# Optimization experiments

Measured on AMD Instinct MI355X. Metric: run time of the kernel, lower is better.

The kernel has to match this reference:

```python
import jax, jax.numpy as jnp
import numpy as np

STATE = 256
HYPER = 256
QHID = 64
NAGENTS = 8


def _lin_init(key, fan_in, fan_out):
    # torch nn.Linear default init: U(-1/sqrt(fan_in), 1/sqrt(fan_in))
    kw, kb = jax.random.split(key)
    bound = 1.0 / np.sqrt(fan_in)
    W = jax.random.uniform(kw, (fan_in, fan_out), jnp.float32, -bound, bound)
    b = jax.random.uniform(kb, (fan_out,), jnp.float32, -bound, bound)
    return W, b


def setup_inputs() -> dict:
    key = jax.random.key(0)
    ks = jax.random.split(key, 8)
    q_value_batch = jax.random.normal(ks[0], (128, 512, NAGENTS, 1), jnp.float32)
    state_batch = jax.random.normal(ks[1], (128, 512, 1, STATE), jnp.float32)
    W1a, b1a = _lin_init(ks[2], STATE, HYPER)
    W1b, b1b = _lin_init(ks[3], HYPER, NAGENTS * QHID)
    W2a, b2a = _lin_init(ks[4], STATE, HYPER)
    W2b, b2b = _lin_init(ks[5], HYPER, QHID)
    Wb1, bb1 = _lin_init(ks[6], STATE, QHID)
    kb2a, kb2b = jax.random.split(ks[7])
    Wb2a, bb2a = _lin_init(kb2a, STATE, QHID)
    Wb2b, bb2b = _lin_init(kb2b, QHID, 1)
    return {
        "q_value_batch": q_value_batch, "state_batch": state_batch,
        "W1a": W1a, "b1a": b1a, "W1b": W1b, "b1b": b1b,
        "W2a": W2a, "b2a": b2a, "W2b": W2b, "b2b": b2b,
        "Wb1": Wb1, "bb1": bb1,
        "Wb2a": Wb2a, "bb2a": bb2a, "Wb2b": Wb2b, "bb2b": bb2b,
    }


def reference(q_value_batch, state_batch,
              W1a, b1a, W1b, b1b,
              W2a, b2a, W2b, b2b,
              Wb1, bb1, Wb2a, bb2a, Wb2b, bb2b):
    B = q_value_batch.shape[0]
    # flatten (num_episode, episode_limit) -> N
    q = q_value_batch.reshape(-1, 1, NAGENTS)          # [N, 1, A]
    s = state_batch.reshape(-1, STATE)                 # [N, S]
    # hypernet w1: S -> H -> A*Q, abs
    w1 = jnp.abs(jax.nn.relu(s @ W1a + b1a) @ W1b + b1b)
    w1 = w1.reshape(-1, NAGENTS, QHID)                 # [N, A, Q]
    b1 = (s @ Wb1 + bb1)[:, None, :]                   # [N, 1, Q]
    hidden = jax.nn.elu(jnp.einsum('nxa,naq->nxq', q, w1) + b1)  # [N, 1, Q]
    # hypernet w2: S -> H -> Q, abs
    w2 = jnp.abs(jax.nn.relu(s @ W2a + b2a) @ W2b + b2b)[:, :, None]  # [N, Q, 1]
    b2 = (jax.nn.relu(s @ Wb2a + bb2a) @ Wb2b + bb2b)[:, :, None]     # [N, 1, 1]
    q_total = jnp.einsum('nxq,nqo->nxo', hidden, w2) + b2             # [N, 1, 1]
    return q_total.reshape(B, -1, 1)
```

## Files before the change

### kernel.cpp

```cpp
#include <hip/hip_runtime.h>

typedef __bf16 bf16_t;
typedef bf16_t bf16x8 __attribute__((ext_vector_type(8)));
typedef bf16_t bf16x4 __attribute__((ext_vector_type(4)));
typedef bf16_t bf16x2 __attribute__((ext_vector_type(2)));
typedef float f32x4 __attribute__((ext_vector_type(4)));

#define MFMA __builtin_amdgcn_mfma_f32_16x16x32_bf16
#define SWZ(row, off) ((off) ^ (((row) & 7) << 4))

#define OFF_W1AT   0
#define OFF_W2AT   65536
#define OFF_W1BT   131072
#define OFF_SMALLT 262144
#define OFF_W2BT   294912
#define OFF_W2OUT  622592ul
#define OFF_B1ROW  9011200ul
#define OFF_B2OUT  17399808ul

__device__ __forceinline__ bf16x8 cvt8(float4 a, float4 b) {
  bf16x8 v;
  v[0]=(bf16_t)a.x; v[1]=(bf16_t)a.y; v[2]=(bf16_t)a.z; v[3]=(bf16_t)a.w;
  v[4]=(bf16_t)b.x; v[5]=(bf16_t)b.y; v[6]=(bf16_t)b.z; v[7]=(bf16_t)b.w;
  return v;
}

__global__ __launch_bounds__(256) void cvt_wT(
    const float* __restrict__ W1a, const float* __restrict__ W2a,
    const float* __restrict__ W1b, const float* __restrict__ Wb1,
    const float* __restrict__ Wb2a, const float* __restrict__ W2b,
    bf16_t* __restrict__ ws)
{
  int gid = blockIdx.x * 256 + threadIdx.x;
  const float* src; int base, nout;
  if (gid < 65536)       { src = W1a;  base = 0;      nout = 256; }
  else if (gid < 131072) { src = W2a;  base = 65536;  nout = 256; }
  else if (gid < 262144) { src = W1b;  base = 131072; nout = 512; }
  else if (gid < 278528) { src = Wb1;  base = 262144; nout = 64;  }
  else if (gid < 294912) { src = Wb2a; base = 278528; nout = 64;  }
  else                   { src = W2b;  base = 294912; nout = 64;  }
  int local = gid - base, col = local >> 8, k = local & 255;
  ws[gid] = (bf16_t)src[k * nout + col];
}

__global__ __launch_bounds__(512) void qmix_k1(
    const float* __restrict__ s, const bf16_t* __restrict__ ws,
    const float* __restrict__ b2a, const float* __restrict__ b2b,
    const float* __restrict__ bb1, const float* __restrict__ bb2a,
    const float* __restrict__ Wb2b, const float* __restrict__ bb2b,
    bf16_t* __restrict__ w2out, bf16_t* __restrict__ b1row,
    float* __restrict__ b2out)
{
  __shared__ __align__(16) char ldsV[64 * 512];
  __shared__ __align__(16) char sT[2][16 * 512];
  __shared__ __align__(16) char h2T[16 * 512];
  __shared__ float b2part[4][16];

  const int tid = threadIdx.x, wave = tid >> 6, lane = tid & 63;
  const int r16 = lane & 15, g = lane >> 4;
  const int row0 = blockIdx.x * 128;
  const int srow = tid >> 5, sc = tid & 31;

  bf16x8 aW[2][8], aSm[8];
  {
    const bf16_t* w2aT = ws + OFF_W2AT;
    const bf16_t* smT  = ws + OFF_SMALLT;
    #pragma unroll
    for (int t = 0; t < 2; ++t) {
      int col = (wave + t * 8) * 16 + r16;
      #pragma unroll
      for (int kk = 0; kk < 8; ++kk)
        aW[t][kk] = *(const bf16x8*)(w2aT + col * 256 + kk * 32 + g * 8);
    }
    int scol = wave * 16 + r16;
    #pragma unroll
    for (int kk = 0; kk < 8; ++kk)
      aSm[kk] = *(const bf16x8*)(smT + scol * 256 + kk * 32 + g * 8);
  }
  {
    const char* src = (const char*)(ws + OFF_W2BT);
    for (int c = tid; c < 2048; c += 512) {
      int col = c >> 5, o = (c & 31) * 16;
      *(float4*)(&ldsV[col * 512 + SWZ(col, o)]) = *(const float4*)(src + c * 16);
    }
  }
  {
    const float* p = s + (size_t)(row0 + srow) * 256 + sc * 8;
    float4 f0 = *(const float4*)p, f1 = *(const float4*)(p + 4);
    *(bf16x8*)(&sT[0][srow * 512 + SWZ(srow, sc * 16)]) = cvt8(f0, f1);
  }
  __syncthreads();

  for (int rt = 0; rt < 8; ++rt) {
    const int cur = rt & 1;
    const int rowt = row0 + rt * 16;
    float4 pf0, pf1;
    if (rt < 7) {
      const float* p = s + (size_t)(rowt + 16 + srow) * 256 + sc * 8;
      pf0 = *(const float4*)p; pf1 = *(const float4*)(p + 4);
    }
    f32x4 acc0 = (f32x4)0.f, acc1 = (f32x4)0.f, accS = (f32x4)0.f;
    #pragma unroll
    for (int kk = 0; kk < 8; ++kk) {
      bf16x8 sB = *(const bf16x8*)(&sT[cur][r16 * 512 + SWZ(r16, kk * 64 + g * 16)]);
      acc0 = MFMA(aW[0][kk], sB, acc0, 0, 0, 0);
      acc1 = MFMA(aW[1][kk], sB, acc1, 0, 0, 0);
      accS = MFMA(aSm[kk], sB, accS, 0, 0, 0);
    }
    if (wave < 4) {
      float4 bb = *(const float4*)(bb1 + wave * 16 + 4 * g);
      bf16x4 o;
      o[0]=(bf16_t)(accS[0]+bb.x); o[1]=(bf16_t)(accS[1]+bb.y);
      o[2]=(bf16_t)(accS[2]+bb.z); o[3]=(bf16_t)(accS[3]+bb.w);
      *(bf16x4*)(b1row + (size_t)(rowt + r16) * 64 + wave * 16 + 4 * g) = o;
    } else {
      float4 ba = *(const float4*)(bb2a + (wave - 4) * 16 + 4 * g);
      float4 wv = *(const float4*)(Wb2b + (wave - 4) * 16 + 4 * g);
      float part = fmaxf(accS[0]+ba.x,0.f)*wv.x + fmaxf(accS[1]+ba.y,0.f)*wv.y
                 + fmaxf(accS[2]+ba.z,0.f)*wv.z + fmaxf(accS[3]+ba.w,0.f)*wv.w;
      part += __shfl_xor(part, 16); part += __shfl_xor(part, 32);
      if (lane < 16) b2part[wave - 4][r16] = part;
    }
    {
      float4 b0 = *(const float4*)(b2a + wave * 16 + 4 * g);
      bf16x4 h;
      h[0]=(bf16_t)fmaxf(acc0[0]+b0.x,0.f); h[1]=(bf16_t)fmaxf(acc0[1]+b0.y,0.f);
      h[2]=(bf16_t)fmaxf(acc0[2]+b0.z,0.f); h[3]=(bf16_t)fmaxf(acc0[3]+b0.w,0.f);
      *(bf16x4*)(&h2T[r16 * 512 + SWZ(r16, wave * 32 + 8 * g)]) = h;
      float4 b1_ = *(const float4*)(b2a + 128 + wave * 16 + 4 * g);
      bf16x4 h2;
      h2[0]=(bf16_t)fmaxf(acc1[0]+b1_.x,0.f); h2[1]=(bf16_t)fmaxf(acc1[1]+b1_.y,0.f);
      h2[2]=(bf16_t)fmaxf(acc1[2]+b1_.z,0.f); h2[3]=(bf16_t)fmaxf(acc1[3]+b1_.w,0.f);
      *(bf16x4*)(&h2T[r16 * 512 + SWZ(r16, 256 + wave * 32 + 8 * g)]) = h2;
    }
    __syncthreads();
    if (rt < 7)
      *(bf16x8*)(&sT[cur ^ 1][srow * 512 + SWZ(srow, sc * 16)]) = cvt8(pf0, pf1);
    if (wave < 4) {
      f32x4 accV = (f32x4)0.f;
      const int vcol = wave * 16 + r16;
      #pragma unroll
      for (int kk = 0; kk < 8; ++kk) {
        bf16x8 hB = *(const bf16x8*)(&h2T[r16 * 512 + SWZ(r16, kk * 64 + g * 16)]);
        bf16x8 aV = *(const bf16x8*)(&ldsV[vcol * 512 + SWZ(vcol, kk * 64 + g * 16)]);
        accV = MFMA(aV, hB, accV, 0, 0, 0);
      }
      float4 bv = *(const float4*)(b2b + wave * 16 + 4 * g);
      bf16x4 o;
      o[0]=(bf16_t)fabsf(accV[0]+bv.x); o[1]=(bf16_t)fabsf(accV[1]+bv.y);
      o[2]=(bf16_t)fabsf(accV[2]+bv.z); o[3]=(bf16_t)fabsf(accV[3]+bv.w);
      *(bf16x4*)(w2out + (size_t)(rowt + r16) * 64 + wave * 16 + 4 * g) = o;
    } else if (wave == 7 && lane < 16) {
      b2out[rowt + lane] = b2part[0][lane] + b2part[1][lane]
                         + b2part[2][lane] + b2part[3][lane] + bb2b[0];
    }
    __syncthreads();
  }
}

__global__ __launch_bounds__(512) void qmix_k2(
    const float* __restrict__ s, const float* __restrict__ q,
    const bf16_t* __restrict__ ws,
    const float* __restrict__ b1a, const float* __restrict__ b1b,
    const bf16_t* __restrict__ w2in, const bf16_t* __restrict__ b1row,
    const float* __restrict__ b2in, float* __restrict__ out)
{
  __shared__ __align__(16) char ldsA[128 * 512];
  __shared__ __align__(16) char sT[2][16 * 512];
  __shared__ __align__(16) char h1T[16 * 512];
  __shared__ __align__(16) char slab[8 * 4096];

  const int tid = threadIdx.x, wave = tid >> 6, lane = tid & 63;
  const int r16 = lane & 15, g = lane >> 4;
  const int row0 = blockIdx.x * 128;
  const int srow = tid >> 5, sc = tid & 31;

  bf16x8 aB[4][8], aA[8];
  {
    const bf16_t* w1bT = ws + OFF_W1BT;
    #pragma unroll
    for (int tt = 0; tt < 4; ++tt)
      #pragma unroll
      for (int kk = 0; kk < 8; ++kk)
        aB[tt][kk] = *(const bf16x8*)(w1bT + (wave * 64 + tt * 16 + r16) * 256 + kk * 32 + g * 8);
    #pragma unroll
    for (int kk = 0; kk < 8; ++kk)
      aA[kk] = *(const bf16x8*)(ws + (wave * 16 + r16) * 256 + kk * 32 + g * 8);
  }
  {
    const char* srcA = (const char*)(ws + 128 * 256);
    for (int c = tid; c < 4096; c += 512) {
      int col = c >> 5, o = (c & 31) * 16;
      *(float4*)(&ldsA[col * 512 + SWZ(col, o)]) = *(const float4*)(srcA + c * 16);
    }
  }
  {
    const float* p = s + (size_t)(row0 + srow) * 256 + sc * 8;
    float4 f0 = *(const float4*)p, f1 = *(const float4*)(p + 4);
    *(bf16x8*)(&sT[0][srow * 512 + SWZ(srow, sc * 16)]) = cvt8(f0, f1);
  }
  __syncthreads();

  for (int rt = 0; rt < 8; ++rt) {
    const int cur = rt & 1;
    const int rowt = row0 + rt * 16;
    float4 pf0, pf1;
    if (rt < 7) {
      const float* p = s + (size_t)(rowt + 16 + srow) * 256 + sc * 8;
      pf0 = *(const float4*)p; pf1 = *(const float4*)(p + 4);
    }
    float qa = q[(size_t)(rowt + r16) * 8 + wave];
    f32x4 acc0 = (f32x4)0.f, acc1 = (f32x4)0.f;
    const int lcol = wave * 16 + r16;
    #pragma unroll
    for (int kk = 0; kk < 8; ++kk) {
      bf16x8 sB = *(const bf16x8*)(&sT[cur][r16 * 512 + SWZ(r16, kk * 64 + g * 16)]);
      acc0 = MFMA(aA[kk], sB, acc0, 0, 0, 0);
      bf16x8 aL = *(const bf16x8*)(&ldsA[lcol * 512 + SWZ(lcol, kk * 64 + g * 16)]);
      acc1 = MFMA(aL, sB, acc1, 0, 0, 0);
    }
    {
      float4 b0 = *(const float4*)(b1a + wave * 16 + 4 * g);
      bf16x4 h;
      h[0]=(bf16_t)fmaxf(acc0[0]+b0.x,0.f); h[1]=(bf16_t)fmaxf(acc0[1]+b0.y,0.f);
      h[2]=(bf16_t)fmaxf(acc0[2]+b0.z,0.f); h[3]=(bf16_t)fmaxf(acc0[3]+b0.w,0.f);
      *(bf16x4*)(&h1T[r16 * 512 + SWZ(r16, wave * 32 + 8 * g)]) = h;
      float4 b1_ = *(const float4*)(b1a + 128 + wave * 16 + 4 * g);
      bf16x4 h2;
      h2[0]=(bf16_t)fmaxf(acc1[0]+b1_.x,0.f); h2[1]=(bf16_t)fmaxf(acc1[1]+b1_.y,0.f);
      h2[2]=(bf16_t)fmaxf(acc1[2]+b1_.z,0.f); h2[3]=(bf16_t)fmaxf(acc1[3]+b1_.w,0.f);
      *(bf16x4*)(&h1T[r16 * 512 + SWZ(r16, 256 + wave * 32 + 8 * g)]) = h2;
    }
    __syncthreads();
    if (rt < 7)
      *(bf16x8*)(&sT[cur ^ 1][srow * 512 + SWZ(srow, sc * 16)]) = cvt8(pf0, pf1);
    f32x4 a2[4];
    #pragma unroll
    for (int tt = 0; tt < 4; ++tt) a2[tt] = (f32x4)0.f;
    #pragma unroll
    for (int kk = 0; kk < 8; ++kk) {
      bf16x8 hB = *(const bf16x8*)(&h1T[r16 * 512 + SWZ(r16, kk * 64 + g * 16)]);
      #pragma unroll
      for (int tt = 0; tt < 4; ++tt)
        a2[tt] = MFMA(aB[tt][kk], hB, a2[tt], 0, 0, 0);
    }
    #pragma unroll
    for (int tt = 0; tt < 4; ++tt) {
      float4 bb = *(const float4*)(b1b + wave * 64 + tt * 16 + 4 * g);
      f32x4 v;
      v[0]=qa*fabsf(a2[tt][0]+bb.x); v[1]=qa*fabsf(a2[tt][1]+bb.y);
      v[2]=qa*fabsf(a2[tt][2]+bb.z); v[3]=qa*fabsf(a2[tt][3]+bb.w);
      *(f32x4*)(&slab[wave * 4096 + r16 * 256 + SWZ(r16, (tt * 16 + 4 * g) * 4)]) = v;
    }
    __syncthreads();
    {
      int row = srow, qp = sc * 2;
      float s0 = 0.f, s1 = 0.f;
      #pragma unroll
      for (int w = 0; w < 8; ++w) {
        float2 sv = *(const float2*)(&slab[w * 4096 + row * 256 + SWZ(row, qp * 4)]);
        s0 += sv.x; s1 += sv.y;
      }
      bf16x2 bv = *(const bf16x2*)(b1row + (size_t)(rowt + row) * 64 + qp);
      float h0 = s0 + (float)bv[0], h1 = s1 + (float)bv[1];
      h0 = h0 > 0.f ? h0 : (__expf(h0) - 1.f);
      h1 = h1 > 0.f ? h1 : (__expf(h1) - 1.f);
      bf16x2 wv = *(const bf16x2*)(w2in + (size_t)(rowt + row) * 64 + qp);
      float dot = h0 * (float)wv[0] + h1 * (float)wv[1];
      dot += __shfl_xor(dot, 1); dot += __shfl_xor(dot, 2);
      dot += __shfl_xor(dot, 4); dot += __shfl_xor(dot, 8);
      dot += __shfl_xor(dot, 16);
      if (sc == 0) out[rowt + row] = dot + b2in[rowt + row];
    }
  }
}

extern "C" void kernel_launch(void* const* d_in, const int* in_sizes, int n_in,
                              void* d_out, int out_size, void* d_ws, size_t ws_size,
                              hipStream_t stream) {
  const float* q    = (const float*)d_in[0];
  const float* s    = (const float*)d_in[1];
  const float* W1a  = (const float*)d_in[2];
  const float* b1a  = (const float*)d_in[3];
  const float* W1b  = (const float*)d_in[4];
  const float* b1b  = (const float*)d_in[5];
  const float* W2a  = (const float*)d_in[6];
  const float* b2a  = (const float*)d_in[7];
  const float* W2b  = (const float*)d_in[8];
  const float* b2b  = (const float*)d_in[9];
  const float* Wb1  = (const float*)d_in[10];
  const float* bb1  = (const float*)d_in[11];
  const float* Wb2a = (const float*)d_in[12];
  const float* bb2a = (const float*)d_in[13];
  const float* Wb2b = (const float*)d_in[14];
  const float* bb2b = (const float*)d_in[15];
  bf16_t* ws = (bf16_t*)d_ws;
  float* out = (float*)d_out;

  bf16_t* w2out = (bf16_t*)((char*)d_ws + OFF_W2OUT);
  bf16_t* b1row = (bf16_t*)((char*)d_ws + OFF_B1ROW);
  float*  b2out = (float*)((char*)d_ws + OFF_B2OUT);

  int N  = in_sizes[0] / 8;
  int nb = N / 128;

  cvt_wT<<<1216, 256, 0, stream>>>(W1a, W2a, W1b, Wb1, Wb2a, W2b, ws);
  qmix_k1<<<nb, 512, 0, stream>>>(s, ws, b2a, b2b, bb1, bb2a, Wb2b, bb2b,
                                  w2out, b1row, b2out);
  qmix_k2<<<nb, 512, 0, stream>>>(s, q, ws, b1a, b1b, w2out, b1row,
                                  b2out, out);
}
```

Baseline: 114.3 us.

## Split second hypernet kernel, process 32-row tiles, and atomically accumulate b2

After: 168.5 us. 1.47x slower.

```diff
diff --git a/kernel.cpp b/kernel.cpp
--- a/kernel.cpp
+++ b/kernel.cpp
@@ -3,7 +3,6 @@
 typedef __bf16 bf16_t;
 typedef bf16_t bf16x8 __attribute__((ext_vector_type(8)));
 typedef bf16_t bf16x4 __attribute__((ext_vector_type(4)));
-typedef bf16_t bf16x2 __attribute__((ext_vector_type(2)));
 typedef float f32x4 __attribute__((ext_vector_type(4)));
 
 #define MFMA __builtin_amdgcn_mfma_f32_16x16x32_bf16
@@ -17,6 +16,7 @@
 #define OFF_W2OUT  622592ul
 #define OFF_B1ROW  9011200ul
 #define OFF_B2OUT  17399808ul
+#define OFF_H1     17661952ul
 
 __device__ __forceinline__ bf16x8 cvt8(float4 a, float4 b) {
   bf16x8 v;
@@ -29,9 +29,14 @@
     const float* __restrict__ W1a, const float* __restrict__ W2a,
     const float* __restrict__ W1b, const float* __restrict__ Wb1,
     const float* __restrict__ Wb2a, const float* __restrict__ W2b,
-    bf16_t* __restrict__ ws)
+    bf16_t* __restrict__ ws, float* __restrict__ b2out)
 {
   int gid = blockIdx.x * 256 + threadIdx.x;
+  if (gid >= 311296) {
+    int i = gid - 311296;
+    b2out[i] = 0.f;
+    return;
+  }
   const float* src; int base, nout;
   if (gid < 65536)       { src = W1a;  base = 0;      nout = 256; }
   else if (gid < 131072) { src = W2a;  base = 65536;  nout = 256; }
@@ -43,7 +48,7 @@
   ws[gid] = (bf16_t)src[k * nout + col];
 }
 
-__global__ __launch_bounds__(512) void qmix_k1(
+__global__ __launch_bounds__(512, 4) void qmix_k1(
     const float* __restrict__ s, const bf16_t* __restrict__ ws,
     const float* __restrict__ b2a, const float* __restrict__ b2b,
     const float* __restrict__ bb1, const float* __restrict__ bb2a,
@@ -52,30 +57,20 @@
     float* __restrict__ b2out)
 {
   __shared__ __align__(16) char ldsV[64 * 512];
-  __shared__ __align__(16) char sT[2][16 * 512];
-  __shared__ __align__(16) char h2T[16 * 512];
-  __shared__ float b2part[4][16];
-
+  __shared__ __align__(16) char sT[2][32 * 512];
+  __shared__ __align__(16) char h2T[32 * 512];
   const int tid = threadIdx.x, wave = tid >> 6, lane = tid & 63;
   const int r16 = lane & 15, g = lane >> 4;
   const int row0 = blockIdx.x * 128;
-  const int srow = tid >> 5, sc = tid & 31;
-
-  bf16x8 aW[2][8], aSm[8];
-  {
-    const bf16_t* w2aT = ws + OFF_W2AT;
-    const bf16_t* smT  = ws + OFF_SMALLT;
-    #pragma unroll
-    for (int t = 0; t < 2; ++t) {
-      int col = (wave + t * 8) * 16 + r16;
-      #pragma unroll
-      for (int kk = 0; kk < 8; ++kk)
-        aW[t][kk] = *(const bf16x8*)(w2aT + col * 256 + kk * 32 + g * 8);
-    }
-    int scol = wave * 16 + r16;
+  const int srow = tid >> 4, sc = tid & 15;
+
+  bf16x8 aW[2][8];
+  #pragma unroll
+  for (int t = 0; t < 2; ++t) {
+    int col = (wave + t * 8) * 16 + r16;
     #pragma unroll
     for (int kk = 0; kk < 8; ++kk)
-      aSm[kk] = *(const bf16x8*)(smT + scol * 256 + kk * 32 + g * 8);
+      aW[t][kk] = *(const bf16x8*)(ws + OFF_W2AT + col * 256 + kk * 32 + g * 8);
   }
   {
     const char* src = (const char*)(ws + OFF_W2BT);
@@ -85,193 +80,259 @@
     }
   }
   {
-    const float* p = s + (size_t)(row0 + srow) * 256 + sc * 8;
-    float4 f0 = *(const float4*)p, f1 = *(const float4*)(p + 4);
-    *(bf16x8*)(&sT[0][srow * 512 + SWZ(srow, sc * 16)]) = cvt8(f0, f1);
+    const float* p = s + (size_t)(row0 + srow) * 256 + sc * 16;
+    *(bf16x8*)(&sT[0][srow * 512 + SWZ(srow, sc * 32)]) =
+        cvt8(((const float4*)p)[0], ((const float4*)p)[1]);
+    *(bf16x8*)(&sT[0][srow * 512 + SWZ(srow, sc * 32 + 16)]) =
+        cvt8(((const float4*)p)[2], ((const float4*)p)[3]);
   }
   __syncthreads();
 
-  for (int rt = 0; rt < 8; ++rt) {
+  const float bb2b0 = bb2b[0];
+  for (int rt = 0; rt < 4; ++rt) {
     const int cur = rt & 1;
-    const int rowt = row0 + rt * 16;
-    float4 pf0, pf1;
-    if (rt < 7) {
-      const float* p = s + (size_t)(rowt + 16 + srow) * 256 + sc * 8;
-      pf0 = *(const float4*)p; pf1 = *(const float4*)(p + 4);
-    }
-    f32x4 acc0 = (f32x4)0.f, acc1 = (f32x4)0.f, accS = (f32x4)0.f;
+    const int rowt = row0 + rt * 32;
+    float4 pf0, pf1, pf2, pf3;
+    if (rt < 3) {
+      const float* p = s + (size_t)(rowt + 32 + srow) * 256 + sc * 16;
+      pf0 = ((const float4*)p)[0]; pf1 = ((const float4*)p)[1];
+      pf2 = ((const float4*)p)[2]; pf3 = ((const float4*)p)[3];
+    }
+    f32x4 acc[2][2], accS[2];
+    #pragma unroll
+    for (int t = 0; t < 2; ++t) { acc[t][0] = (f32x4)0.f; acc[t][1] = (f32x4)0.f; }
+    accS[0] = (f32x4)0.f; accS[1] = (f32x4)0.f;
+
     #pragma unroll
     for (int kk = 0; kk < 8; ++kk) {
-      bf16x8 sB = *(const bf16x8*)(&sT[cur][r16 * 512 + SWZ(r16, kk * 64 + g * 16)]);
-      acc0 = MFMA(aW[0][kk], sB, acc0, 0, 0, 0);
-      acc1 = MFMA(aW[1][kk], sB, acc1, 0, 0, 0);
-      accS = MFMA(aSm[kk], sB, accS, 0, 0, 0);
+      bf16x8 aS = *(const bf16x8*)(ws + OFF_SMALLT + (wave * 16 + r16) * 256 + kk * 32 + g * 8);
+      #pragma unroll
+      for (int h = 0; h < 2; ++h) {
+        int rr = h * 16 + r16;
+        bf16x8 sB = *(const bf16x8*)(&sT[cur][rr * 512 + SWZ(rr, kk * 64 + g * 16)]);
+        acc[0][h] = MFMA(aW[0][kk], sB, acc[0][h], 0, 0, 0);
+        acc[1][h] = MFMA(aW[1][kk], sB, acc[1][h], 0, 0, 0);
+        accS[h]   = MFMA(aS,        sB, accS[h],   0, 0, 0);
+      }
+    }
+    #pragma unroll
+    for (int t = 0; t < 2; ++t) {
+      float4 b0 = *(const float4*)(b2a + (wave + t * 8) * 16 + 4 * g);
+      #pragma unroll
+      for (int h = 0; h < 2; ++h) {
+        int rr = h * 16 + r16;
+        bf16x4 hv;
+        hv[0] = (bf16_t)fmaxf(acc[t][h][0] + b0.x, 0.f);
+        hv[1] = (bf16_t)fmaxf(acc[t][h][1] + b0.y, 0.f);
+        hv[2] = (bf16_t)fmaxf(acc[t][h][2] + b0.z, 0.f);
+        hv[3] = (bf16_t)fmaxf(acc[t][h][3] + b0.w, 0.f);
+        *(bf16x4*)(&h2T[rr * 512 + SWZ(rr, (wave + t * 8) * 32 + 8 * g)]) = hv;
+      }
     }
     if (wave < 4) {
       float4 bb = *(const float4*)(bb1 + wave * 16 + 4 * g);
-      bf16x4 o;
-      o[0]=(bf16_t)(accS[0]+bb.x); o[1]=(bf16_t)(accS[1]+bb.y);
-      o[2]=(bf16_t)(accS[2]+bb.z); o[3]=(bf16_t)(accS[3]+bb.w);
-      *(bf16x4*)(b1row + (size_t)(rowt + r16) * 64 + wave * 16 + 4 * g) = o;
+      #pragma unroll
+      for (int h = 0; h < 2; ++h) {
+        bf16x4 o;
+        o[0]=(bf16_t)(accS[h][0]+bb.x); o[1]=(bf16_t)(accS[h][1]+bb.y);
+        o[2]=(bf16_t)(accS[h][2]+bb.z); o[3]=(bf16_t)(accS[h][3]+bb.w);
+        *(bf16x4*)(b1row + (size_t)(rowt + h * 16 + r16) * 64 + wave * 16 + 4 * g) = o;
+      }
     } else {
       float4 ba = *(const float4*)(bb2a + (wave - 4) * 16 + 4 * g);
       float4 wv = *(const float4*)(Wb2b + (wave - 4) * 16 + 4 * g);
-      float part = fmaxf(accS[0]+ba.x,0.f)*wv.x + fmaxf(accS[1]+ba.y,0.f)*wv.y
-                 + fmaxf(accS[2]+ba.z,0.f)*wv.z + fmaxf(accS[3]+ba.w,0.f)*wv.w;
-      part += __shfl_xor(part, 16); part += __shfl_xor(part, 32);
-      if (lane < 16) b2part[wave - 4][r16] = part;
-    }
+      #pragma unroll
+      for (int h = 0; h < 2; ++h) {
+        float part = fmaxf(accS[h][0]+ba.x,0.f)*wv.x + fmaxf(accS[h][1]+ba.y,0.f)*wv.y
+                   + fmaxf(accS[h][2]+ba.z,0.f)*wv.z + fmaxf(accS[h][3]+ba.w,0.f)*wv.w;
+        part += __shfl_xor(part, 16); part += __shfl_xor(part, 32);
+        if (lane < 16) {
+          float add = part + (wave == 4 ? bb2b0 : 0.f);
+          atomicAdd(&b2out[rowt + h * 16 + r16], add);
+        }
+      }
+    }
+    if (rt < 3) {
+      *(bf16x8*)(&sT[cur ^ 1][srow * 512 + SWZ(srow, sc * 32)])      = cvt8(pf0, pf1);
+      *(bf16x8*)(&sT[cur ^ 1][srow * 512 + SWZ(srow, sc * 32 + 16)]) = cvt8(pf2, pf3);
+    }
+    __syncthreads();
     {
-      float4 b0 = *(const float4*)(b2a + wave * 16 + 4 * g);
-      bf16x4 h;
-      h[0]=(bf16_t)fmaxf(acc0[0]+b0.x,0.f); h[1]=(bf16_t)fmaxf(acc0[1]+b0.y,0.f);
-      h[2]=(bf16_t)fmaxf(acc0[2]+b0.z,0.f); h[3]=(bf16_t)fmaxf(acc0[3]+b0.w,0.f);
-      *(bf16x4*)(&h2T[r16 * 512 + SWZ(r16, wave * 32 + 8 * g)]) = h;
-      float4 b1_ = *(const float4*)(b2a + 128 + wave * 16 + 4 * g);
-      bf16x4 h2;
-      h2[0]=(bf16_t)fmaxf(acc1[0]+b1_.x,0.f); h2[1]=(bf16_t)fmaxf(acc1[1]+b1_.y,0.f);
-      h2[2]=(bf16_t)fmaxf(acc1[2]+b1_.z,0.f); h2[3]=(bf16_t)fmaxf(acc1[3]+b1_.w,0.f);
-      *(bf16x4*)(&h2T[r16 * 512 + SWZ(r16, 256 + wave * 32 + 8 * g)]) = h2;
-    }
-    __syncthreads();
-    if (rt < 7)
-      *(bf16x8*)(&sT[cur ^ 1][srow * 512 + SWZ(srow, sc * 16)]) = cvt8(pf0, pf1);
-    if (wave < 4) {
+      const int ct = wave >> 1, h = wave & 1, rr = h * 16 + r16;
+      const int vc = ct * 16 + r16;
       f32x4 accV = (f32x4)0.f;
-      const int vcol = wave * 16 + r16;
       #pragma unroll
       for (int kk = 0; kk < 8; ++kk) {
-        bf16x8 hB = *(const bf16x8*)(&h2T[r16 * 512 + SWZ(r16, kk * 64 + g * 16)]);
-        bf16x8 aV = *(const bf16x8*)(&ldsV[vcol * 512 + SWZ(vcol, kk * 64 + g * 16)]);
+        bf16x8 hB = *(const bf16x8*)(&h2T[rr * 512 + SWZ(rr, kk * 64 + g * 16)]);
+        bf16x8 aV = *(const bf16x8*)(&ldsV[vc * 512 + SWZ(vc, kk * 64 + g * 16)]);
         accV = MFMA(aV, hB, accV, 0, 0, 0);
       }
-      float4 bv = *(const float4*)(b2b + wave * 16 + 4 * g);
+      float4 bv = *(const float4*)(b2b + ct * 16 + 4 * g);
       bf16x4 o;
       o[0]=(bf16_t)fabsf(accV[0]+bv.x); o[1]=(bf16_t)fabsf(accV[1]+bv.y);
       o[2]=(bf16_t)fabsf(accV[2]+bv.z); o[3]=(bf16_t)fabsf(accV[3]+bv.w);
-      *(bf16x4*)(w2out + (size_t)(rowt + r16) * 64 + wave * 16 + 4 * g) = o;
-    } else if (wave == 7 && lane < 16) {
-      b2out[rowt + lane] = b2part[0][lane] + b2part[1][lane]
-                         + b2part[2][lane] + b2part[3][lane] + bb2b[0];
-    }
-    __syncthreads();
-  }
-}
-
-__global__ __launch_bounds__(512) void qmix_k2(
-    const float* __restrict__ s, const float* __restrict__ q,
-    const bf16_t* __restrict__ ws,
-    const float* __restrict__ b1a, const float* __restrict__ b1b,
+      *(bf16x4*)(w2out + (size_t)(rowt + h * 16 + r16) * 64 + ct * 16 + 4 * g) = o;
+    }
+    __syncthreads();
+  }
+}
+
+__global__ __launch_bounds__(512, 4) void qmix_k2a(
+    const float* __restrict__ s, const bf16_t* __restrict__ ws,
+    const float* __restrict__ b1a, bf16_t* __restrict__ h1g)
+{
+  __shared__ __align__(16) char sT[2][32 * 512];
+  const int tid = threadIdx.x, wave = tid >> 6, lane = tid & 63;
+  const int r16 = lane & 15, g = lane >> 4;
+  const int row0 = blockIdx.x * 128;
+  const int srow = tid >> 4, sc = tid & 15;
+
+  bf16x8 aA[2][8];
+  #pragma unroll
+  for (int t = 0; t < 2; ++t) {
+    int col = (wave + t * 8) * 16 + r16;
+    #pragma unroll
+    for (int kk = 0; kk < 8; ++kk)
+      aA[t][kk] = *(const bf16x8*)(ws + OFF_W1AT + col * 256 + kk * 32 + g * 8);
+  }
+  {
+    const float* p = s + (size_t)(row0 + srow) * 256 + sc * 16;
+    *(bf16x8*)(&sT[0][srow * 512 + SWZ(srow, sc * 32)]) =
+        cvt8(((const float4*)p)[0], ((const float4*)p)[1]);
+    *(bf16x8*)(&sT[0][srow * 512 + SWZ(srow, sc * 32 + 16)]) =
+        cvt8(((const float4*)p)[2], ((const float4*)p)[3]);
+  }
+  __syncthreads();
+
+  for (int rt = 0; rt < 4; ++rt) {
+    const int cur = rt & 1;
+    const int rowt = row0 + rt * 32;
+    float4 pf0, pf1, pf2, pf3;
+    if (rt < 3) {
+      const float* p = s + (size_t)(rowt + 32 + srow) * 256 + sc * 16;
+      pf0 = ((const float4*)p)[0]; pf1 = ((const float4*)p)[1];
+      pf2 = ((const float4*)p)[2]; pf3 = ((const float4*)p)[3];
+    }
+    f32x4 acc[2][2];
+    #pragma unroll
+    for (int t = 0; t < 2; ++t) { acc[t][0] = (f32x4)0.f; acc[t][1] = (f32x4)0.f; }
+    #pragma unroll
+    for (int kk = 0; kk < 8; ++kk) {
+      #pragma unroll
+      for (int h = 0; h < 2; ++h) {
+        int rr = h * 16 + r16;
+        bf16x8 sB = *(const bf16x8*)(&sT[cur][rr * 512 + SWZ(rr, kk * 64 + g * 16)]);
+        acc[0][h] = MFMA(aA[0][kk], sB, acc[0][h], 0, 0, 0);
+        acc[1][h] = MFMA(aA[1][kk], sB, acc[1][h], 0, 0, 0);
+      }
+    }
+    #pragma unroll
+    for (int t = 0; t < 2; ++t) {
+      float4 b0 = *(const float4*)(b1a + (wave + t * 8) * 16 + 4 * g);
+      #pragma unroll
+      for (int h = 0; h < 2; ++h) {
+        bf16x4 hv;
+        hv[0] = (bf16_t)fmaxf(acc[t][h][0] + b0.x, 0.f);
+        hv[1] = (bf16_t)fmaxf(acc[t][h][1] + b0.y, 0.f);
+        hv[2] = (bf16_t)fmaxf(acc[t][h][2] + b0.z, 0.f);
+        hv[3] = (bf16_t)fmaxf(acc[t][h][3] + b0.w, 0.f);
+        *(bf16x4*)(h1g + (size_t)(rowt + h * 16 + r16) * 256 + (wave + t * 8) * 16 + 4 * g) = hv;
+      }
+    }
+    if (rt < 3) {
+      *(bf16x8*)(&sT[cur ^ 1][srow * 512 + SWZ(srow, sc * 32)])      = cvt8(pf0, pf1);
+      *(bf16x8*)(&sT[cur ^ 1][srow * 512 + SWZ(srow, sc * 32 + 16)]) = cvt8(pf2, pf3);
+    }
+    __syncthreads();
+  }
+}
+
+__global__ __launch_bounds__(512, 4) void qmix_k2b(
+    const float* __restrict__ q, const bf16_t* __restrict__ ws,
+    const float* __restrict__ b1b, const bf16_t* __restrict__ h1g,
     const bf16_t* __restrict__ w2in, const bf16_t* __restrict__ b1row,
     const float* __restrict__ b2in, float* __restrict__ out)
 {
-  __shared__ __align__(16) char ldsA[128 * 512];
-  __shared__ __align__(16) char sT[2][16 * 512];
-  __shared__ __align__(16) char h1T[16 * 512];
-  __shared__ __align__(16) char slab[8 * 4096];
-
+  __shared__ __align__(16) char slab[8 * 8192];
   const int tid = threadIdx.x, wave = tid >> 6, lane = tid & 63;
   const int r16 = lane & 15, g = lane >> 4;
   const int row0 = blockIdx.x * 128;
-  const int srow = tid >> 5, sc = tid & 31;
-
-  bf16x8 aB[4][8], aA[8];
-  {
-    const bf16_t* w1bT = ws + OFF_W1BT;
-    #pragma unroll
-    for (int tt = 0; tt < 4; ++tt)
-      #pragma unroll
-      for (int kk = 0; kk < 8; ++kk)
-        aB[tt][kk] = *(const bf16x8*)(w1bT + (wave * 64 + tt * 16 + r16) * 256 + kk * 32 + g * 8);
+
+  bf16x8 aB[2][8];
+  #pragma unroll
+  for (int tt = 0; tt < 2; ++tt) {
+    int col = wave * 64 + tt * 16 + r16;
     #pragma unroll
     for (int kk = 0; kk < 8; ++kk)
-      aA[kk] = *(const bf16x8*)(ws + (wave * 16 + r16) * 256 + kk * 32 + g * 8);
-  }
-  {
-    const char* srcA = (const char*)(ws + 128 * 256);
-    for (int c = tid; c < 4096; c += 512) {
-      int col = c >> 5, o = (c & 31) * 16;
-      *(float4*)(&ldsA[col * 512 + SWZ(col, o)]) = *(const float4*)(srcA + c * 16);
-    }
-  }
-  {
-    const float* p = s + (size_t)(row0 + srow) * 256 + sc * 8;
-    float4 f0 = *(const float4*)p, f1 = *(const float4*)(p + 4);
-    *(bf16x8*)(&sT[0][srow * 512 + SWZ(srow, sc * 16)]) = cvt8(f0, f1);
-  }
-  __syncthreads();
-
-  for (int rt = 0; rt < 8; ++rt) {
-    const int cur = rt & 1;
-    const int rowt = row0 + rt * 16;
-    float4 pf0, pf1;
-    if (rt < 7) {
-      const float* p = s + (size_t)(rowt + 16 + srow) * 256 + sc * 8;
-      pf0 = *(const float4*)p; pf1 = *(const float4*)(p + 4);
-    }
-    float qa = q[(size_t)(rowt + r16) * 8 + wave];
-    f32x4 acc0 = (f32x4)0.f, acc1 = (f32x4)0.f;
-    const int lcol = wave * 16 + r16;
+      aB[tt][kk] = *(const bf16x8*)(ws + OFF_W1BT + col * 256 + kk * 32 + g * 8);
+  }
+
+  for (int rt = 0; rt < 4; ++rt) {
+    const int rowt = row0 + rt * 32;
+    float qa0 = q[(size_t)(rowt + r16) * 8 + wave];
+    float qa1 = q[(size_t)(rowt + 16 + r16) * 8 + wave];
+    f32x4 a2[4][2];
+    #pragma unroll
+    for (int tt = 0; tt < 4; ++tt) { a2[tt][0] = (f32x4)0.f; a2[tt][1] = (f32x4)0.f; }
+
+    const bf16_t* hbase0 = h1g + (size_t)(rowt + r16) * 256 + g * 8;
+    const bf16_t* hbase1 = h1g + (size_t)(rowt + 16 + r16) * 256 + g * 8;
+    bf16x8 nb0 = *(const bf16x8*)(hbase0);
+    bf16x8 nb1 = *(const bf16x8*)(hbase1);
     #pragma unroll
     for (int kk = 0; kk < 8; ++kk) {
-      bf16x8 sB = *(const bf16x8*)(&sT[cur][r16 * 512 + SWZ(r16, kk * 64 + g * 16)]);
-      acc0 = MFMA(aA[kk], sB, acc0, 0, 0, 0);
-      bf16x8 aL = *(const bf16x8*)(&ldsA[lcol * 512 + SWZ(lcol, kk * 64 + g * 16)]);
-      acc1 = MFMA(aL, sB, acc1, 0, 0, 0);
-    }
-    {
-      float4 b0 = *(const float4*)(b1a + wave * 16 + 4 * g);
-      bf16x4 h;
-      h[0]=(bf16_t)fmaxf(acc0[0]+b0.x,0.f); h[1]=(bf16_t)fmaxf(acc0[1]+b0.y,0.f);
-      h[2]=(bf16_t)fmaxf(acc0[2]+b0.z,0.f); h[3]=(bf16_t)fmaxf(acc0[3]+b0.w,0.f);
-      *(bf16x4*)(&h1T[r16 * 512 + SWZ(r16, wave * 32 + 8 * g)]) = h;
-      float4 b1_ = *(const float4*)(b1a + 128 + wave * 16 + 4 * g);
-      bf16x4 h2;
-      h2[0]=(bf16_t)fmaxf(acc1[0]+b1_.x,0.f); h2[1]=(bf16_t)fmaxf(acc1[1]+b1_.y,0.f);
-      h2[2]=(bf16_t)fmaxf(acc1[2]+b1_.z,0.f); h2[3]=(bf16_t)fmaxf(acc1[3]+b1_.w,0.f);
-      *(bf16x4*)(&h1T[r16 * 512 + SWZ(r16, 256 + wave * 32 + 8 * g)]) = h2;
-    }
-    __syncthreads();
-    if (rt < 7)
-      *(bf16x8*)(&sT[cur ^ 1][srow * 512 + SWZ(srow, sc * 16)]) = cvt8(pf0, pf1);
-    f32x4 a2[4];
-    #pragma unroll
-    for (int tt = 0; tt < 4; ++tt) a2[tt] = (f32x4)0.f;
-    #pragma unroll
-    for (int kk = 0; kk < 8; ++kk) {
-      bf16x8 hB = *(const bf16x8*)(&h1T[r16 * 512 + SWZ(r16, kk * 64 + g * 16)]);
-      #pragma unroll
-      for (int tt = 0; tt < 4; ++tt)
-        a2[tt] = MFMA(aB[tt][kk], hB, a2[tt], 0, 0, 0);
+      bf16x8 hb0 = nb0, hb1 = nb1;
+      if (kk < 7) {
+        nb0 = *(const bf16x8*)(hbase0 + (kk + 1) * 32);
+        nb1 = *(const bf16x8*)(hbase1 + (kk + 1) * 32);
+      }
+      a2[0][0] = MFMA(aB[0][kk], hb0, a2[0][0], 0, 0, 0);
+      a2[0][1] = MFMA(aB[0][kk], hb1, a2[0][1], 0, 0, 0);
+      a2[1][0] = MFMA(aB[1][kk], hb0, a2[1][0], 0, 0, 0);
+      a2[1][1] = MFMA(aB[1][kk], hb1, a2[1][1], 0, 0, 0);
+      bf16x8 w2f = *(const bf16x8*)(ws + OFF_W1BT + (wave * 64 + 32 + r16) * 256 + kk * 32 + g * 8);
+      a2[2][0] = MFMA(w2f, hb0, a2[2][0], 0, 0, 0);
+      a2[2][1] = MFMA(w2f, hb1, a2[2][1], 0, 0, 0);
+      bf16x8 w3f = *(const bf16x8*)(ws + OFF_W1BT + (wave * 64 + 48 + r16) * 256 + kk * 32 + g * 8);
+      a2[3][0] = MFMA(w3f, hb0, a2[3][0], 0, 0, 0);
+      a2[3][1] = MFMA(w3f, hb1, a2[3][1], 0, 0, 0);
     }
     #pragma unroll
     for (int tt = 0; tt < 4; ++tt) {
       float4 bb = *(const float4*)(b1b + wave * 64 + tt * 16 + 4 * g);
-      f32x4 v;
-      v[0]=qa*fabsf(a2[tt][0]+bb.x); v[1]=qa*fabsf(a2[tt][1]+bb.y);
-      v[2]=qa*fabsf(a2[tt][2]+bb.z); v[3]=qa*fabsf(a2[tt][3]+bb.w);
-      *(f32x4*)(&slab[wave * 4096 + r16 * 256 + SWZ(r16, (tt * 16 + 4 * g) * 4)]) = v;
+      #pragma unroll
+      for (int h = 0; h < 2; ++h) {
+        float qa = h ? qa1 : qa0;
+        int rr = h * 16 + r16;
+        f32x4 v;
+        v[0] = qa * fabsf(a2[tt][h][0] + bb.x);
+        v[1] = qa * fabsf(a2[tt][h][1] + bb.y);
+        v[2] = qa * fabsf(a2[tt][h][2] + bb.z);
+        v[3] = qa * fabsf(a2[tt][h][3] + bb.w);
+        *(f32x4*)(&slab[wave * 8192 + rr * 256 + SWZ(rr, (tt * 16 + 4 * g) * 4)]) = v;
+      }
     }
     __syncthreads();
     {
-      int row = srow, qp = sc * 2;
-      float s0 = 0.f, s1 = 0.f;
-      #pragma unroll
-      for (int w = 0; w < 8; ++w) {
-        float2 sv = *(const float2*)(&slab[w * 4096 + row * 256 + SWZ(row, qp * 4)]);
-        s0 += sv.x; s1 += sv.y;
-      }
-      bf16x2 bv = *(const bf16x2*)(b1row + (size_t)(rowt + row) * 64 + qp);
-      float h0 = s0 + (float)bv[0], h1 = s1 + (float)bv[1];
-      h0 = h0 > 0.f ? h0 : (__expf(h0) - 1.f);
-      h1 = h1 > 0.f ? h1 : (__expf(h1) - 1.f);
-      bf16x2 wv = *(const bf16x2*)(w2in + (size_t)(rowt + row) * 64 + qp);
-      float dot = h0 * (float)wv[0] + h1 * (float)wv[1];
+      int row = tid >> 4, qi = (tid & 15) * 4;
+      f32x4 sum = (f32x4)0.f;
+      #pragma unroll
+      for (int a = 0; a < 8; ++a)
+        sum += *(const f32x4*)(&slab[a * 8192 + row * 256 + SWZ(row, qi * 4)]);
+      bf16x4 b1v = *(const bf16x4*)(b1row + (size_t)(rowt + row) * 64 + qi);
+      bf16x4 w2v = *(const bf16x4*)(w2in + (size_t)(rowt + row) * 64 + qi);
+      float dot = 0.f;
+      #pragma unroll
+      for (int e = 0; e < 4; ++e) {
+        float hh = sum[e] + (float)b1v[e];
+        hh = hh > 0.f ? hh : (__expf(hh) - 1.f);
+        dot += hh * (float)w2v[e];
+      }
       dot += __shfl_xor(dot, 1); dot += __shfl_xor(dot, 2);
       dot += __shfl_xor(dot, 4); dot += __shfl_xor(dot, 8);
-      dot += __shfl_xor(dot, 16);
-      if (sc == 0) out[rowt + row] = dot + b2in[rowt + row];
-    }
+      if ((tid & 15) == 0) out[rowt + row] = dot + b2in[rowt + row];
+    }
+    __syncthreads();
   }
 }
 
@@ -300,13 +361,14 @@
   bf16_t* w2out = (bf16_t*)((char*)d_ws + OFF_W2OUT);
   bf16_t* b1row = (bf16_t*)((char*)d_ws + OFF_B1ROW);
   float*  b2out = (float*)((char*)d_ws + OFF_B2OUT);
+  bf16_t* h1g   = (bf16_t*)((char*)d_ws + OFF_H1);
 
   int N  = in_sizes[0] / 8;
   int nb = N / 128;
 
-  cvt_wT<<<1216, 256, 0, stream>>>(W1a, W2a, W1b, Wb1, Wb2a, W2b, ws);
+  cvt_wT<<<1472, 256, 0, stream>>>(W1a, W2a, W1b, Wb1, Wb2a, W2b, ws, b2out);
   qmix_k1<<<nb, 512, 0, stream>>>(s, ws, b2a, b2b, bb1, bb2a, Wb2b, bb2b,
                                   w2out, b1row, b2out);
-  qmix_k2<<<nb, 512, 0, stream>>>(s, q, ws, b1a, b1b, w2out, b1row,
-                                  b2out, out);
-}
+  qmix_k2a<<<nb, 512, 0, stream>>>(s, ws, b1a, h1g);
+  qmix_k2b<<<nb, 512, 0, stream>>>(q, ws, b1b, h1g, w2out, b1row, b2out, out);
+}
```
